# Kernel optimization log

Hardware: AMD Instinct MI355X
Metric: run time of the kernel (lower is better)

The kernel has to match this reference:

```python
import jax, jax.numpy as jnp
import numpy as np

N_NODES = 50000
N_EDGES = 800000
IN_DIM = 128
OUT_DIM = 64
NEG_SLOPE = 0.01  # torch F.leaky_relu default


def setup_inputs() -> dict:
    key = jax.random.key(0)
    k1, k2, k3, k4, k5 = jax.random.split(key, 5)
    features = jax.random.normal(k1, (N_NODES, IN_DIM), dtype=jnp.float32)
    # xavier-ish scale for weights
    fc_w = jax.random.normal(k2, (OUT_DIM, IN_DIM), dtype=jnp.float32) * (1.0 / np.sqrt(IN_DIM))
    attn_w = jax.random.normal(k3, (2 * OUT_DIM,), dtype=jnp.float32) * (1.0 / np.sqrt(2 * OUT_DIM))
    src = jax.random.randint(k4, (N_EDGES,), 0, N_NODES, dtype=jnp.int32)
    dst = jax.random.randint(k5, (N_EDGES,), 0, N_NODES, dtype=jnp.int32)
    return {"features": features, "fc_w": fc_w, "attn_w": attn_w, "src": src, "dst": dst}


def reference(features, fc_w, attn_w, src, dst):
    n = features.shape[0]
    out_dim = fc_w.shape[0]
    # z = fc(features), [N, out_dim]
    z = features @ fc_w.T
    # attn_fc([z_src || z_dst]) = z_src @ w_src + z_dst @ w_dst
    a_src = z @ attn_w[:out_dim]   # [N]
    a_dst = z @ attn_w[out_dim:]   # [N]
    e = a_src[src] + a_dst[dst]    # [E] per-edge raw score
    e = jnp.where(e > 0, e, NEG_SLOPE * e)  # leaky_relu
    # edge softmax over incoming edges of each dst node
    e_max = jax.ops.segment_max(e, dst, num_segments=n)      # [N]
    w = jnp.exp(e - e_max[dst])                               # [E]
    denom = jax.ops.segment_sum(w, dst, num_segments=n)       # [N]
    # weighted neighbor sum: sum_e alpha_e * z[src_e]
    num = jax.ops.segment_sum(w[:, None] * z[src], dst, num_segments=n)  # [N, out_dim]
    h = num / jnp.where(denom > 0, denom, 1.0)[:, None]
    # activation = elu
    h = jax.nn.elu(h)
    return h
```

## Files before the change

### kernel.cpp

```cpp
#include <hip/hip_runtime.h>
#include <hip/hip_bf16.h>
#include <hip/hip_fp16.h>

#define N_NODES 50000
#define N_EDGES 800000
#define IN_DIM 128
#define OUT_DIM 64
#define NEG_SLOPE 0.01f
#define NEG_INF (-3.0e38f)

#define N_STRIPS (N_NODES / 16)
#define Z_BLOCKS ((N_STRIPS + 3) / 4)
#define E_I4 (N_EDGES / 4)

#define NB ((N_NODES + 127) / 128)
#define CAP_B 3072
#define CNT_STRIDE 16
#define EB 200
#define CHUNK_I4 (E_I4 / EB)

typedef __bf16 bf16x8 __attribute__((ext_vector_type(8)));
typedef float f32x4 __attribute__((ext_vector_type(4)));

__device__ __forceinline__ unsigned short f2bf_us(float f) {
  __hip_bfloat16 h = __float2bfloat16(f);
  return *reinterpret_cast<unsigned short*>(&h);
}
__device__ __forceinline__ bf16x8 pack_bf16(float4 lo, float4 hi) {
  union { bf16x8 v; unsigned short u[8]; } r;
  r.u[0] = f2bf_us(lo.x); r.u[1] = f2bf_us(lo.y);
  r.u[2] = f2bf_us(lo.z); r.u[3] = f2bf_us(lo.w);
  r.u[4] = f2bf_us(hi.x); r.u[5] = f2bf_us(hi.y);
  r.u[6] = f2bf_us(hi.z); r.u[7] = f2bf_us(hi.w);
  return r.v;
}
__device__ __forceinline__ float bflo(unsigned u) {
  return __uint_as_float(u << 16);
}
__device__ __forceinline__ float bfhi(unsigned u) {
  return __uint_as_float(u & 0xffff0000u);
}

__global__ __launch_bounds__(256) void gat_z_bucket(
    const float* __restrict__ feat, const float* __restrict__ fcw,
    const float* __restrict__ attnw, __hip_bfloat16* __restrict__ z,
    float* __restrict__ asrc, float* __restrict__ adst,
    const int* __restrict__ src, const int* __restrict__ dst,
    int* __restrict__ cnt, unsigned* __restrict__ pairs) {
  if (blockIdx.x >= Z_BLOCKS) {
    __shared__ int hist[NB];
    __shared__ int curs[NB];
    const int tid = threadIdx.x;
    const int i0 = (blockIdx.x - Z_BLOCKS) * CHUNK_I4;
    for (int i = tid; i < NB; i += 256) hist[i] = 0;
    __syncthreads();
    for (int t = i0 + tid; t < i0 + CHUNK_I4; t += 256) {
      int4 d = ((const int4*)dst)[t];
      atomicAdd(&hist[d.x >> 7], 1);
      atomicAdd(&hist[d.y >> 7], 1);
      atomicAdd(&hist[d.z >> 7], 1);
      atomicAdd(&hist[d.w >> 7], 1);
    }
    __syncthreads();
    for (int i = tid; i < NB; i += 256) {
      int h = hist[i];
      curs[i] = h ? atomicAdd(cnt + i * CNT_STRIDE, h) : 0;
    }
    __syncthreads();
    for (int t = i0 + tid; t < i0 + CHUNK_I4; t += 256) {
      int4 s = ((const int4*)src)[t];
      int4 d = ((const int4*)dst)[t];
#define BKT_PUT(dd, ss)                                                    \
  {                                                                        \
    int b = (dd) >> 7;                                                     \
    int r = atomicAdd(&curs[b], 1);                                        \
    if (r < CAP_B)                                                         \
      pairs[(size_t)b * CAP_B + r] =                                       \
          ((unsigned)((dd) & 127) << 16) | (unsigned)(ss);                 \
  }
      BKT_PUT(d.x, s.x)
      BKT_PUT(d.y, s.y)
      BKT_PUT(d.z, s.z)
      BKT_PUT(d.w, s.w)
#undef BKT_PUT
    }
    return;
  }

  const int lane = threadIdx.x & 63;
  const int m = lane & 15;
  const int quad = lane >> 4;
  const int wv = blockIdx.x * 4 + (threadIdx.x >> 6);
  if (wv >= N_STRIPS) return;
  const int n0 = wv * 16;

  bf16x8 bfrag[4][4];
#pragma unroll
  for (int t = 0; t < 4; ++t) {
    const float* wr = fcw + (size_t)(m + 16 * t) * IN_DIM + quad * 8;
#pragma unroll
    for (int c = 0; c < 4; ++c) {
      float4 lo = *(const float4*)(wr + c * 32);
      float4 hi = *(const float4*)(wr + c * 32 + 4);
      bfrag[t][c] = pack_bf16(lo, hi);
    }
  }

  f32x4 acc[4] = {{0.f, 0.f, 0.f, 0.f}, {0.f, 0.f, 0.f, 0.f},
                  {0.f, 0.f, 0.f, 0.f}, {0.f, 0.f, 0.f, 0.f}};
  const float* ar = feat + (size_t)(n0 + m) * IN_DIM + quad * 8;
#pragma unroll
  for (int c = 0; c < 4; ++c) {
    float4 lo = *(const float4*)(ar + c * 32);
    float4 hi = *(const float4*)(ar + c * 32 + 4);
    const bf16x8 af = pack_bf16(lo, hi);
#pragma unroll
    for (int t = 0; t < 4; ++t)
      acc[t] = __builtin_amdgcn_mfma_f32_16x16x32_bf16(af, bfrag[t][c],
                                                       acc[t], 0, 0, 0);
  }

#pragma unroll
  for (int t = 0; t < 4; ++t)
#pragma unroll
    for (int r = 0; r < 4; ++r)
      z[(size_t)(n0 + quad * 4 + r) * OUT_DIM + m + 16 * t] =
          __float2bfloat16(acc[t][r]);

  float aws[4], awd[4];
#pragma unroll
  for (int t = 0; t < 4; ++t) {
    aws[t] = attnw[m + 16 * t];
    awd[t] = attnw[OUT_DIM + m + 16 * t];
  }
  float ps[4], pd[4];
#pragma unroll
  for (int r = 0; r < 4; ++r) {
    float s = 0.f, d = 0.f;
#pragma unroll
    for (int t = 0; t < 4; ++t) {
      s = fmaf(acc[t][r], aws[t], s);
      d = fmaf(acc[t][r], awd[t], d);
    }
    ps[r] = s;
    pd[r] = d;
  }
#pragma unroll
  for (int off = 1; off < 16; off <<= 1) {
#pragma unroll
    for (int r = 0; r < 4; ++r) {
      ps[r] += __shfl_xor(ps[r], off, 64);
      pd[r] += __shfl_xor(pd[r], off, 64);
    }
  }
  if (m == 0) {
#pragma unroll
    for (int r = 0; r < 4; ++r) {
      asrc[n0 + quad * 4 + r] = ps[r];
      adst[n0 + quad * 4 + r] = pd[r];
    }
  }
}

__global__ __launch_bounds__(512) void gat_csr_agg(
    const unsigned* __restrict__ pairs, const int* __restrict__ cnt,
    const __hip_bfloat16* __restrict__ zb, const float* __restrict__ asrc,
    const float* __restrict__ adst, float* __restrict__ out) {
  __shared__ int hist[32];
  __shared__ int noff[33];
  __shared__ int cur[32];
  __shared__ int lsrc[CAP_B];
  const int tid = threadIdx.x;
  const int b = blockIdx.x >> 2;
  const int q = blockIdx.x & 3;
  const int c = min(cnt[b * CNT_STRIDE], CAP_B);
  const unsigned* __restrict__ bp = pairs + (size_t)b * CAP_B;

  if (tid < 32) hist[tid] = 0;
  __syncthreads();
  for (int i = tid; i < c; i += 512) {
    const int ln = (int)(bp[i] >> 16);
    if ((ln >> 5) == q) atomicAdd(&hist[ln & 31], 1);
  }
  __syncthreads();
  if (tid < 32) {
    const int h = hist[tid];
    int s = h;
#pragma unroll
    for (int off = 1; off < 32; off <<= 1) {
      const int u = __shfl_up(s, off, 64);
      if (tid >= off) s += u;
    }
    noff[tid] = s - h;
    cur[tid] = s - h;
    if (tid == 31) noff[32] = s;
  }
  __syncthreads();
  for (int i = tid; i < c; i += 512) {
    const unsigned p = bp[i];
    const int ln = (int)(p >> 16);
    if ((ln >> 5) == q) {
      const int r = atomicAdd(&cur[ln & 31], 1);
      lsrc[r] = (int)(p & 0xFFFFu);
    }
  }
  __syncthreads();

  const int lane = tid & 63;
  const int wv = tid >> 6;
  const int g = lane >> 4;
  const int sl = lane & 15;
  const int j2 = sl & 3;
  const int eg = sl >> 2;
  const int gbase = lane & 48;

  const int ln = wv * 4 + g;
  const int node = b * 128 + q * 32 + ln;
  if (node >= N_NODES) return;

  const uint4* __restrict__ zp4 = (const uint4*)zb;
  const int o0 = noff[ln];
  const int o1 = noff[ln + 1];
  float4* __restrict__ orow = (float4*)(out + (size_t)node * OUT_DIM);
  if (o0 == o1) {
    if (sl < 4) {
      const float4 zv = {0.f, 0.f, 0.f, 0.f};
#pragma unroll
      for (int v = 0; v < 4; ++v) orow[4 * sl + v] = zv;
    }
    return;
  }
  const float ad = adst[node];

  float m = NEG_INF, dsum = 0.f;
  float acc[16];
#pragma unroll
  for (int cc = 0; cc < 16; ++cc) acc[cc] = 0.f;

  for (int base = o0; base < o1; base += 16) {
    const int cnt2 = min(16, o1 - base);
    int s = 0;
    float ev = NEG_INF;
    if (sl < cnt2) {
      s = lsrc[base + sl];
      const float v = asrc[s] + ad;
      ev = v > 0.f ? v : NEG_SLOPE * v;
    }
    float cm = ev;
#pragma unroll
    for (int off = 1; off < 16; off <<= 1)
      cm = fmaxf(cm, __shfl_xor(cm, off, 64));
    const float nm = fmaxf(m, cm);
    const float scale = __expf(m - nm);
    dsum *= scale;
#pragma unroll
    for (int cc = 0; cc < 16; ++cc) acc[cc] *= scale;
    m = nm;

    const float w = (sl < cnt2) ? __expf(ev - m) : 0.f;
    dsum += w;
    const unsigned pk =
        (unsigned)s |
        ((unsigned)__half_as_ushort(__float2half(w)) << 16);

    const int ngr = (cnt2 + 3) >> 2;
    for (int gg = 0; gg < ngr; ++gg) {
      const unsigned pa = __shfl(pk, gbase + 4 * gg + eg, 64);
      const int sa = (int)(pa & 0xFFFFu);
      const float wa =
          __half2float(__ushort_as_half((unsigned short)(pa >> 16)));
      const uint4 ua = zp4[(size_t)sa * 8 + 2 * j2];
      const uint4 ub = zp4[(size_t)sa * 8 + 2 * j2 + 1];
      acc[0] = fmaf(wa, bflo(ua.x), acc[0]);
      acc[1] = fmaf(wa, bfhi(ua.x), acc[1]);
      acc[2] = fmaf(wa, bflo(ua.y), acc[2]);
      acc[3] = fmaf(wa, bfhi(ua.y), acc[3]);
      acc[4] = fmaf(wa, bflo(ua.z), acc[4]);
      acc[5] = fmaf(wa, bfhi(ua.z), acc[5]);
      acc[6] = fmaf(wa, bflo(ua.w), acc[6]);
      acc[7] = fmaf(wa, bfhi(ua.w), acc[7]);
      acc[8] = fmaf(wa, bflo(ub.x), acc[8]);
      acc[9] = fmaf(wa, bfhi(ub.x), acc[9]);
      acc[10] = fmaf(wa, bflo(ub.y), acc[10]);
      acc[11] = fmaf(wa, bfhi(ub.y), acc[11]);
      acc[12] = fmaf(wa, bflo(ub.z), acc[12]);
      acc[13] = fmaf(wa, bfhi(ub.z), acc[13]);
      acc[14] = fmaf(wa, bflo(ub.w), acc[14]);
      acc[15] = fmaf(wa, bfhi(ub.w), acc[15]);
    }
  }

#pragma unroll
  for (int off = 4; off <= 8; off <<= 1)
#pragma unroll
    for (int cc = 0; cc < 16; ++cc) acc[cc] += __shfl_xor(acc[cc], off, 64);
#pragma unroll
  for (int off = 1; off < 16; off <<= 1) dsum += __shfl_xor(dsum, off, 64);

  if (eg == 0) {
    const float inv = 1.f / (dsum > 0.f ? dsum : 1.f);
#pragma unroll
    for (int v = 0; v < 4; ++v) {
      float4 r;
      float h;
      h = acc[4 * v + 0] * inv; r.x = h > 0.f ? h : expm1f(h);
      h = acc[4 * v + 1] * inv; r.y = h > 0.f ? h : expm1f(h);
      h = acc[4 * v + 2] * inv; r.z = h > 0.f ? h : expm1f(h);
      h = acc[4 * v + 3] * inv; r.w = h > 0.f ? h : expm1f(h);
      orow[4 * j2 + v] = r;
    }
  }
}

extern "C" void kernel_launch(void* const* d_in, const int* in_sizes, int n_in,
                              void* d_out, int out_size, void* d_ws, size_t ws_size,
                              hipStream_t stream) {
  const float* feat  = (const float*)d_in[0];
  const float* fcw   = (const float*)d_in[1];
  const float* attnw = (const float*)d_in[2];
  const int* src     = (const int*)d_in[3];
  const int* dst     = (const int*)d_in[4];
  float* out = (float*)d_out;

  char* ws = (char*)d_ws;
  __hip_bfloat16* z = (__hip_bfloat16*)ws;
  ws += (size_t)N_NODES * OUT_DIM * sizeof(__hip_bfloat16);
  float* asrc = (float*)ws;   ws += (size_t)N_NODES * sizeof(float);
  float* adst = (float*)ws;   ws += (size_t)N_NODES * sizeof(float);
  int* cnt = (int*)ws;        ws += (size_t)NB * CNT_STRIDE * sizeof(int);
  unsigned* pairs = (unsigned*)ws; ws += (size_t)NB * CAP_B * sizeof(unsigned);

  hipMemsetAsync(cnt, 0, (size_t)NB * CNT_STRIDE * sizeof(int), stream);

  gat_z_bucket<<<Z_BLOCKS + EB, 256, 0, stream>>>(
      feat, fcw, attnw, z, asrc, adst, src, dst, cnt, pairs);
  gat_csr_agg<<<NB * 4, 512, 0, stream>>>(pairs, cnt, z, asrc, adst, out);
}
```

Before: 133.8 us.

## Bucket edges per 32-node block with global atomics and split kernels

```diff
diff --git a/kernel.cpp b/kernel.cpp
--- a/kernel.cpp
+++ b/kernel.cpp
@@ -12,12 +12,11 @@
 #define N_STRIPS (N_NODES / 16)
 #define Z_BLOCKS ((N_STRIPS + 3) / 4)
 #define E_I4 (N_EDGES / 4)
-
-#define NB ((N_NODES + 127) / 128)
-#define CAP_B 3072
-#define CNT_STRIDE 16
-#define EB 200
-#define CHUNK_I4 (E_I4 / EB)
+#define B_BLOCKS ((E_I4 + 255) / 256)
+
+#define NB4 ((N_NODES + 31) / 32)
+#define CAP4 1024
+#define CSTRIDE 4
 
 typedef __bf16 bf16x8 __attribute__((ext_vector_type(8)));
 typedef float f32x4 __attribute__((ext_vector_type(4)));
@@ -41,52 +40,10 @@
   return __uint_as_float(u & 0xffff0000u);
 }
 
-__global__ __launch_bounds__(256) void gat_z_bucket(
+__global__ __launch_bounds__(256) void gat_z(
     const float* __restrict__ feat, const float* __restrict__ fcw,
     const float* __restrict__ attnw, __hip_bfloat16* __restrict__ z,
-    float* __restrict__ asrc, float* __restrict__ adst,
-    const int* __restrict__ src, const int* __restrict__ dst,
-    int* __restrict__ cnt, unsigned* __restrict__ pairs) {
-  if (blockIdx.x >= Z_BLOCKS) {
-    __shared__ int hist[NB];
-    __shared__ int curs[NB];
-    const int tid = threadIdx.x;
-    const int i0 = (blockIdx.x - Z_BLOCKS) * CHUNK_I4;
-    for (int i = tid; i < NB; i += 256) hist[i] = 0;
-    __syncthreads();
-    for (int t = i0 + tid; t < i0 + CHUNK_I4; t += 256) {
-      int4 d = ((const int4*)dst)[t];
-      atomicAdd(&hist[d.x >> 7], 1);
-      atomicAdd(&hist[d.y >> 7], 1);
-      atomicAdd(&hist[d.z >> 7], 1);
-      atomicAdd(&hist[d.w >> 7], 1);
-    }
-    __syncthreads();
-    for (int i = tid; i < NB; i += 256) {
-      int h = hist[i];
-      curs[i] = h ? atomicAdd(cnt + i * CNT_STRIDE, h) : 0;
-    }
-    __syncthreads();
-    for (int t = i0 + tid; t < i0 + CHUNK_I4; t += 256) {
-      int4 s = ((const int4*)src)[t];
-      int4 d = ((const int4*)dst)[t];
-#define BKT_PUT(dd, ss)                                                    \
-  {                                                                        \
-    int b = (dd) >> 7;                                                     \
-    int r = atomicAdd(&curs[b], 1);                                        \
-    if (r < CAP_B)                                                         \
-      pairs[(size_t)b * CAP_B + r] =                                       \
-          ((unsigned)((dd) & 127) << 16) | (unsigned)(ss);                 \
-  }
-      BKT_PUT(d.x, s.x)
-      BKT_PUT(d.y, s.y)
-      BKT_PUT(d.z, s.z)
-      BKT_PUT(d.w, s.w)
-#undef BKT_PUT
-    }
-    return;
-  }
-
+    float* __restrict__ asrc, float* __restrict__ adst) {
   const int lane = threadIdx.x & 63;
   const int m = lane & 15;
   const int quad = lane >> 4;
@@ -160,6 +117,28 @@
       adst[n0 + quad * 4 + r] = pd[r];
     }
   }
+}
+
+__global__ __launch_bounds__(256) void gat_bucket(
+    const int* __restrict__ src, const int* __restrict__ dst,
+    int* __restrict__ cnt, unsigned* __restrict__ pairs) {
+  const int t = blockIdx.x * 256 + threadIdx.x;
+  if (t >= E_I4) return;
+  const int4 s = ((const int4*)src)[t];
+  const int4 d = ((const int4*)dst)[t];
+#define BKT_PUT(dd, ss)                                                    \
+  {                                                                        \
+    const int nb = (dd) >> 5;                                              \
+    const int r = atomicAdd(cnt + nb * CSTRIDE, 1);                        \
+    if (r < CAP4)                                                          \
+      pairs[((size_t)nb << 10) + r] =                                      \
+          ((unsigned)((dd) & 31) << 16) | (unsigned)(ss);                  \
+  }
+  BKT_PUT(d.x, s.x)
+  BKT_PUT(d.y, s.y)
+  BKT_PUT(d.z, s.z)
+  BKT_PUT(d.w, s.w)
+#undef BKT_PUT
 }
 
 __global__ __launch_bounds__(512) void gat_csr_agg(
@@ -169,19 +148,15 @@
   __shared__ int hist[32];
   __shared__ int noff[33];
   __shared__ int cur[32];
-  __shared__ int lsrc[CAP_B];
+  __shared__ int lsrc[CAP4];
   const int tid = threadIdx.x;
-  const int b = blockIdx.x >> 2;
-  const int q = blockIdx.x & 3;
-  const int c = min(cnt[b * CNT_STRIDE], CAP_B);
-  const unsigned* __restrict__ bp = pairs + (size_t)b * CAP_B;
+  const int b = blockIdx.x;
+  const int c = min(cnt[b * CSTRIDE], CAP4);
+  const unsigned* __restrict__ bp = pairs + ((size_t)b << 10);
 
   if (tid < 32) hist[tid] = 0;
   __syncthreads();
-  for (int i = tid; i < c; i += 512) {
-    const int ln = (int)(bp[i] >> 16);
-    if ((ln >> 5) == q) atomicAdd(&hist[ln & 31], 1);
-  }
+  for (int i = tid; i < c; i += 512) atomicAdd(&hist[bp[i] >> 16], 1);
   __syncthreads();
   if (tid < 32) {
     const int h = hist[tid];
@@ -198,11 +173,8 @@
   __syncthreads();
   for (int i = tid; i < c; i += 512) {
     const unsigned p = bp[i];
-    const int ln = (int)(p >> 16);
-    if ((ln >> 5) == q) {
-      const int r = atomicAdd(&cur[ln & 31], 1);
-      lsrc[r] = (int)(p & 0xFFFFu);
-    }
+    const int r = atomicAdd(&cur[p >> 16], 1);
+    lsrc[r] = (int)(p & 0xFFFFu);
   }
   __syncthreads();
 
@@ -215,7 +187,7 @@
   const int gbase = lane & 48;
 
   const int ln = wv * 4 + g;
-  const int node = b * 128 + q * 32 + ln;
+  const int node = b * 32 + ln;
   if (node >= N_NODES) return;
 
   const uint4* __restrict__ zp4 = (const uint4*)zb;
@@ -327,12 +299,12 @@
   ws += (size_t)N_NODES * OUT_DIM * sizeof(__hip_bfloat16);
   float* asrc = (float*)ws;   ws += (size_t)N_NODES * sizeof(float);
   float* adst = (float*)ws;   ws += (size_t)N_NODES * sizeof(float);
-  int* cnt = (int*)ws;        ws += (size_t)NB * CNT_STRIDE * sizeof(int);
-  unsigned* pairs = (unsigned*)ws; ws += (size_t)NB * CAP_B * sizeof(unsigned);
-
-  hipMemsetAsync(cnt, 0, (size_t)NB * CNT_STRIDE * sizeof(int), stream);
-
-  gat_z_bucket<<<Z_BLOCKS + EB, 256, 0, stream>>>(
-      feat, fcw, attnw, z, asrc, adst, src, dst, cnt, pairs);
-  gat_csr_agg<<<NB * 4, 512, 0, stream>>>(pairs, cnt, z, asrc, adst, out);
-}
+  int* cnt = (int*)ws;        ws += (size_t)NB4 * CSTRIDE * sizeof(int);
+  unsigned* pairs = (unsigned*)ws; ws += (size_t)NB4 * CAP4 * sizeof(unsigned);
+
+  hipMemsetAsync(cnt, 0, (size_t)NB4 * CSTRIDE * sizeof(int), stream);
+
+  gat_bucket<<<B_BLOCKS, 256, 0, stream>>>(src, dst, cnt, pairs);
+  gat_z<<<Z_BLOCKS, 256, 0, stream>>>(feat, fcw, attnw, z, asrc, adst);
+  gat_csr_agg<<<NB4, 512, 0, stream>>>(pairs, cnt, z, asrc, adst, out);
+}
```

Result: slower. 202.3 us (+51.2%).
